# Kernel optimization log

Measured on AMD Instinct MI355X. Metric: run time of the kernel, lower is better.

## Reference

```python
import jax, jax.numpy as jnp
import numpy as np
import math

B, T, C, H = 2, 4096, 512, 8
HD = C // H


def setup_inputs() -> dict:
    key = jax.random.key(0)
    k1, k2, k3 = jax.random.split(key, 3)
    x = jax.random.normal(k1, (B, T, C), dtype=jnp.float32)
    # weights stored as [in, out] so y = x @ W (equivalent to torch Linear with W^T)
    w_qkv = jax.random.normal(k2, (C, 3 * C), dtype=jnp.float32) * (1.0 / math.sqrt(C))
    w_out = jax.random.normal(k3, (C, C), dtype=jnp.float32) * (1.0 / math.sqrt(C))
    return {"x": x, "w_qkv": w_qkv, "w_out": w_out}


def reference(x, w_qkv, w_out):
    Bs, Ts, Cs = x.shape
    qkv = x @ w_qkv                                   # [B,T,3C]
    q, k, v = jnp.split(qkv, 3, axis=-1)
    # [B,H,T,HD]
    q = q.reshape(Bs, Ts, H, HD).transpose(0, 2, 1, 3)
    k = k.reshape(Bs, Ts, H, HD).transpose(0, 2, 1, 3)
    v = v.reshape(Bs, Ts, H, HD).transpose(0, 2, 1, 3)
    scores = jnp.einsum("bhqd,bhkd->bhqk", q, k) / math.sqrt(HD)
    causal = jnp.tril(jnp.ones((Ts, Ts), dtype=bool))
    scores = jnp.where(causal[None, None], scores, -jnp.inf)
    attn = jax.nn.softmax(scores, axis=-1)            # [B,H,T,T]
    out = jnp.einsum("bhqk,bhkd->bhqd", attn, v)      # [B,H,T,HD]
    out = out.transpose(0, 2, 1, 3).reshape(Bs, Ts, Cs)
    return out @ w_out
```

## Files before the change

### kernel.cpp

```cpp
#include <hip/hip_runtime.h>
#include <hip/hip_bf16.h>

typedef __bf16 bf16;
typedef __bf16 bf16x4 __attribute__((ext_vector_type(4)));
typedef __bf16 bf16x8 __attribute__((ext_vector_type(8)));
typedef float f32x4 __attribute__((ext_vector_type(4)));

#define BB 2
#define TT 4096
#define CC 512
#define HH 8
#define HD 64
#define BHD 16
#define M_TOT 8192

#define SCL (0.125f * 1.44269504f)

#define GLDS(gptr, lptr)                                                     \
  __builtin_amdgcn_global_load_lds(                                          \
      (const __attribute__((address_space(1))) void*)(gptr),                 \
      (__attribute__((address_space(3))) void*)(lptr), 16, 0, 0)

__global__ __launch_bounds__(256) void convert_x_kernel(
    const float* __restrict__ X, bf16* __restrict__ Xb) {
  const size_t i0 = ((size_t)blockIdx.x * 256 + threadIdx.x) * 16;
  const float4* p = (const float4*)(X + i0);
#pragma unroll
  for (int c = 0; c < 2; ++c) {
    float4 a = p[c * 2], b = p[c * 2 + 1];
    bf16x8 v;
    v[0] = (bf16)a.x; v[1] = (bf16)a.y; v[2] = (bf16)a.z; v[3] = (bf16)a.w;
    v[4] = (bf16)b.x; v[5] = (bf16)b.y; v[6] = (bf16)b.z; v[7] = (bf16)b.w;
    *(bf16x8*)&Xb[i0 + c * 8] = v;
  }
}

__global__ __launch_bounds__(256) void transpose_w_kernel(
    const float* __restrict__ W, bf16* __restrict__ WT, int K, int N) {
  __shared__ float tile[64][65];
  const int n0 = blockIdx.x * 64, k0 = blockIdx.y * 64;
  const int t = threadIdx.x;
  const int rr = t >> 4, cc4 = (t & 15) * 4;
#pragma unroll
  for (int i = 0; i < 4; ++i) {
    float4 v = *(const float4*)&W[(size_t)(k0 + rr + i * 16) * N + n0 + cc4];
    tile[rr + i * 16][cc4 + 0] = v.x;
    tile[rr + i * 16][cc4 + 1] = v.y;
    tile[rr + i * 16][cc4 + 2] = v.z;
    tile[rr + i * 16][cc4 + 3] = v.w;
  }
  __syncthreads();
#pragma unroll
  for (int i = 0; i < 4; ++i) {
    const int nn = rr + i * 16;
    bf16x4 o;
#pragma unroll
    for (int j = 0; j < 4; ++j) o[j] = (bf16)tile[cc4 + j][nn];
    *(bf16x4*)&WT[(size_t)(n0 + nn) * K + k0 + cc4] = o;
  }
}

__global__ __launch_bounds__(256) void gemm_qkv_kernel(
    const bf16* __restrict__ Xb, const bf16* __restrict__ Wt,
    bf16* __restrict__ qw, bf16* __restrict__ kw, bf16* __restrict__ vw) {
  __shared__ __align__(16) bf16 As[128 * 64];
  __shared__ __align__(16) bf16 Bs[128 * 64];
  const int tid = threadIdx.x;
  const int wid = tid >> 6, lane = tid & 63, ln = lane & 15, hi = lane >> 4;
  const int wr = wid >> 1, wc = wid & 1;
  const int m0 = blockIdx.x * 128, n0 = blockIdx.y * 128;
  const int srow = lane >> 3, srcc = (lane & 7) ^ srow;

  f32x4 acc[4][4] = {};

  for (int k0 = 0; k0 < 512; k0 += 64) {
    __syncthreads();
#pragma unroll
    for (int i = 0; i < 4; ++i) {
      const int rb = 32 * wid + 8 * i;
      GLDS(&Xb[(size_t)(m0 + rb + srow) * 512 + k0 + srcc * 8], &As[rb * 64]);
      GLDS(&Wt[(size_t)(n0 + rb + srow) * 512 + k0 + srcc * 8], &Bs[rb * 64]);
    }
    __syncthreads();

    bf16x8 af[4][2], bfr[4][2];
#pragma unroll
    for (int mi = 0; mi < 4; ++mi) {
      const int row = wr * 64 + mi * 16 + ln, rs = row & 7;
      af[mi][0] = *(const bf16x8*)&As[row * 64 + ((hi ^ rs) * 8)];
      af[mi][1] = *(const bf16x8*)&As[row * 64 + (((4 + hi) ^ rs) * 8)];
    }
#pragma unroll
    for (int ni = 0; ni < 4; ++ni) {
      const int row = wc * 64 + ni * 16 + ln, rs = row & 7;
      bfr[ni][0] = *(const bf16x8*)&Bs[row * 64 + ((hi ^ rs) * 8)];
      bfr[ni][1] = *(const bf16x8*)&Bs[row * 64 + (((4 + hi) ^ rs) * 8)];
    }
#pragma unroll
    for (int mi = 0; mi < 4; ++mi)
#pragma unroll
      for (int ni = 0; ni < 4; ++ni) {
        acc[mi][ni] = __builtin_amdgcn_mfma_f32_16x16x32_bf16(af[mi][0], bfr[ni][0], acc[mi][ni], 0, 0, 0);
        acc[mi][ni] = __builtin_amdgcn_mfma_f32_16x16x32_bf16(af[mi][1], bfr[ni][1], acc[mi][ni], 0, 0, 0);
      }
  }

#pragma unroll
  for (int mi = 0; mi < 4; ++mi) {
    int rowb = m0 + wr * 64 + mi * 16 + hi * 4;
    int b = rowb >> 12, t0 = rowb & 4095;
#pragma unroll
    for (int ni = 0; ni < 4; ++ni) {
      int n = n0 + wc * 64 + ni * 16 + ln;
      int which = n >> 9, c = n & 511, h = c >> 6, d = c & 63;
      if (which == 2) {
        bf16x4 pv;
#pragma unroll
        for (int r = 0; r < 4; ++r) pv[r] = (bf16)acc[mi][ni][r];
        *(bf16x4*)&vw[((size_t)(b * HH + h) * HD + d) * TT + t0] = pv;
      } else {
        bf16* dst = which ? kw : qw;
        const float sc = which ? 1.0f : SCL;
#pragma unroll
        for (int r = 0; r < 4; ++r)
          dst[((size_t)(b * HH + h) * TT + t0 + r) * HD + d] = (bf16)(acc[mi][ni][r] * sc);
      }
    }
  }
}

__global__ __launch_bounds__(256) void attn_piece_kernel(
    const bf16* __restrict__ qw, const bf16* __restrict__ kw,
    const bf16* __restrict__ vt,
    bf16* __restrict__ po, float* __restrict__ pl) {
  __shared__ __align__(16) bf16 Ks[2][64 * 64];
  __shared__ __align__(16) bf16 Vs[2][64 * 64];
  const int tid = threadIdx.x;
  const int wid = tid >> 6, lane = tid & 63, ln = lane & 15, hi = lane >> 4;

  const int pid = blockIdx.x;
  const int pair = pid >> 1, half = pid & 1;
  const int qb = 63 - (pair >> 4);
  const int bh = pair & 15;
  const int ntot = qb + 1;
  const int h0 = (ntot + 1) >> 1;
  const int t0 = half ? h0 : 0;
  const int t1 = half ? ntot : h0;

  if (t0 >= t1) {
    for (int i = tid; i < 4096; i += 256) po[(size_t)pid * 4096 + i] = (bf16)0.f;
    if (tid < 64) pl[pid * 64 + tid] = 0.f;
    return;
  }

  const int q0w = qb * 64 + wid * 16;

  const int lrow8 = lane >> 3, lch = lane & 7;
  const int srcch = lch ^ lrow8;
  const int rbase = 8 * wid + lrow8;
  const size_t kb = (size_t)bh * TT * HD, vb = (size_t)bh * HD * TT;

  bf16x8 qf[2];
#pragma unroll
  for (int h = 0; h < 2; ++h)
    qf[h] = *(const bf16x8*)&qw[((size_t)bh * TT + q0w + ln) * HD + h * 32 + hi * 8];

  f32x4 o[4] = {};
  f32x4 osum = {};

  bf16x8 vones;
#pragma unroll
  for (int j = 0; j < 8; ++j) vones[j] = (bf16)1.0f;

#define STAGE(kv_, dstbuf) do {                                              \
    GLDS(kw + kb + (size_t)((kv_) + rbase) * HD + srcch * 8,                 \
         &Ks[dstbuf][(8 * wid) * 64]);                                       \
    GLDS(kw + kb + (size_t)((kv_) + 32 + rbase) * HD + srcch * 8,            \
         &Ks[dstbuf][(32 + 8 * wid) * 64]);                                  \
    GLDS(vt + vb + (size_t)rbase * TT + (kv_) + srcch * 8,                   \
         &Vs[dstbuf][(8 * wid) * 64]);                                       \
    GLDS(vt + vb + (size_t)(32 + rbase) * TT + (kv_) + srcch * 8,            \
         &Vs[dstbuf][(32 + 8 * wid) * 64]);                                  \
  } while (0)

#define TILE(t_, BUF) do {                                                   \
    const int kv0 = (t_) * 64;                                               \
    if ((t_) + 1 < t1) STAGE(kv0 + 64, (BUF) ^ 1);                           \
    f32x4 s[4];                                                              \
    __builtin_amdgcn_s_setprio(1);                                           \
    _Pragma("unroll")                                                        \
    for (int kt = 0; kt < 4; ++kt) {                                         \
      const int krow = kt * 16 + ln;                                         \
      const bf16* kbase = &Ks[BUF][krow * 64];                               \
      bf16x8 kf0 = *(const bf16x8*)&kbase[(hi ^ (ln & 7)) * 8];              \
      bf16x8 kf1 = *(const bf16x8*)&kbase[((4 + hi) ^ (ln & 7)) * 8];        \
      f32x4 a = {};                                                          \
      a = __builtin_amdgcn_mfma_f32_16x16x32_bf16(kf0, qf[0], a, 0, 0, 0);   \
      a = __builtin_amdgcn_mfma_f32_16x16x32_bf16(kf1, qf[1], a, 0, 0, 0);   \
      s[kt] = a;                                                             \
    }                                                                        \
    __builtin_amdgcn_s_setprio(0);                                           \
    if ((t_) == qb) {                                                        \
      const int qg = q0w + ln;                                               \
      _Pragma("unroll")                                                      \
      for (int kt = 0; kt < 4; ++kt)                                         \
        _Pragma("unroll")                                                    \
        for (int r = 0; r < 4; ++r)                                          \
          if (kv0 + kt * 16 + hi * 4 + r > qg) s[kt][r] = -1e30f;            \
    }                                                                        \
    _Pragma("unroll")                                                        \
    for (int kt = 0; kt < 4; ++kt)                                           \
      _Pragma("unroll")                                                      \
      for (int r = 0; r < 4; ++r) s[kt][r] = exp2f(s[kt][r]);                \
    bf16x8 pa[2];                                                            \
    _Pragma("unroll")                                                        \
    for (int h2 = 0; h2 < 2; ++h2)                                           \
      _Pragma("unroll")                                                      \
      for (int j = 0; j < 8; ++j)                                            \
        pa[h2][j] = (bf16)s[h2 * 2 + (j >> 2)][j & 3];                       \
    const bf16* vbase = Vs[BUF];                                             \
    __builtin_amdgcn_s_setprio(1);                                           \
    osum = __builtin_amdgcn_mfma_f32_16x16x32_bf16(pa[0], vones, osum, 0, 0, 0); \
    osum = __builtin_amdgcn_mfma_f32_16x16x32_bf16(pa[1], vones, osum, 0, 0, 0); \
    _Pragma("unroll")                                                        \
    for (int db = 0; db < 4; ++db) {                                         \
      const int d = db * 16 + ln, rowb = d * 64, dx = d & 7;                 \
      _Pragma("unroll")                                                      \
      for (int h2 = 0; h2 < 2; ++h2) {                                       \
        const int c1 = h2 * 4 + (hi >> 1);                                   \
        bf16x4 lo = *(const bf16x4*)&vbase[rowb + ((c1 ^ dx) * 8) + (hi & 1) * 4]; \
        bf16x4 hi4 = *(const bf16x4*)&vbase[rowb + (((c1 + 2) ^ dx) * 8) + (hi & 1) * 4]; \
        bf16x8 vf = __builtin_shufflevector(lo, hi4, 0, 1, 2, 3, 4, 5, 6, 7); \
        o[db] = __builtin_amdgcn_mfma_f32_16x16x32_bf16(pa[h2], vf, o[db], 0, 0, 0); \
      }                                                                      \
    }                                                                        \
    __builtin_amdgcn_s_setprio(0);                                           \
    __syncthreads();                                                         \
  } while (0)

  STAGE(t0 * 64, 0);
  __syncthreads();

  int t = t0;
  for (; t + 1 < t1; t += 2) { TILE(t, 0); TILE(t + 1, 1); }
  if (t < t1) TILE(t, 0);

  {
    bf16* ob = po + (size_t)pid * 4096;
#pragma unroll
    for (int db = 0; db < 4; ++db)
#pragma unroll
      for (int r = 0; r < 4; ++r)
        ob[(wid * 16 + hi * 4 + r) * 64 + db * 16 + ln] = (bf16)o[db][r];
    if (ln == 0) {
#pragma unroll
      for (int r = 0; r < 4; ++r)
        pl[pid * 64 + wid * 16 + hi * 4 + r] = osum[r];
    }
  }
#undef TILE
#undef STAGE
}

__global__ __launch_bounds__(256) void attn_combine_kernel(
    const bf16* __restrict__ po, const float* __restrict__ pl,
    bf16* __restrict__ aw) {
  const int cb = blockIdx.x;
  const int qb = 63 - (cb >> 4), bh = cb & 15;
  const int tid = threadIdx.x;
  const int q_ = tid >> 2, dc = (tid & 3) * 16;
  const int pg0 = cb * 2, pg1 = pg0 + 1;

  const float inv = 1.0f / (pl[pg0 * 64 + q_] + pl[pg1 * 64 + q_]);

  const bf16* o0 = po + (size_t)pg0 * 4096 + q_ * 64 + dc;
  const bf16* o1 = po + (size_t)pg1 * 4096 + q_ * 64 + dc;
  bf16* dst = aw + ((size_t)bh * TT + qb * 64 + q_) * 64 + dc;

#pragma unroll
  for (int c = 0; c < 2; ++c) {
    bf16x8 x = *(const bf16x8*)&o0[c * 8];
    bf16x8 y = *(const bf16x8*)&o1[c * 8];
    bf16x8 outv;
#pragma unroll
    for (int j = 0; j < 8; ++j)
      outv[j] = (bf16)(((float)x[j] + (float)y[j]) * inv);
    *(bf16x8*)&dst[c * 8] = outv;
  }
}

__global__ __launch_bounds__(256) void gemm_out_kernel(
    const bf16* __restrict__ A, const bf16* __restrict__ Wot,
    float* __restrict__ out) {
  __shared__ __align__(16) bf16 As[128 * 64];
  __shared__ __align__(16) bf16 Bs[64 * 64];
  const int tid = threadIdx.x;
  const int wid = tid >> 6, lane = tid & 63, ln = lane & 15, hi = lane >> 4;
  const int wr = wid >> 1, wc = wid & 1;
  const int m0 = blockIdx.x * 128, n0 = blockIdx.y * 64;
  const int srow = lane >> 3, srcc = (lane & 7) ^ srow;

  f32x4 acc[4][2] = {};

  for (int k0 = 0; k0 < 512; k0 += 64) {
    const int h = k0 >> 6;
    __syncthreads();
#pragma unroll
    for (int i = 0; i < 4; ++i) {
      const int rb = 32 * wid + 8 * i;
      const int m = m0 + rb + srow;
      const int b = m >> 12, t = m & 4095;
      GLDS(&A[((size_t)(b * HH + h) * TT + t) * HD + srcc * 8], &As[rb * 64]);
    }
#pragma unroll
    for (int i = 0; i < 2; ++i) {
      const int rb = 16 * wid + 8 * i;
      GLDS(&Wot[(size_t)(n0 + rb + srow) * 512 + k0 + srcc * 8], &Bs[rb * 64]);
    }
    __syncthreads();

    bf16x8 af[4][2], bfr[2][2];
#pragma unroll
    for (int mi = 0; mi < 4; ++mi) {
      const int row = wr * 64 + mi * 16 + ln, rs = row & 7;
      af[mi][0] = *(const bf16x8*)&As[row * 64 + ((hi ^ rs) * 8)];
      af[mi][1] = *(const bf16x8*)&As[row * 64 + (((4 + hi) ^ rs) * 8)];
    }
#pragma unroll
    for (int ni = 0; ni < 2; ++ni) {
      const int row = wc * 32 + ni * 16 + ln, rs = row & 7;
      bfr[ni][0] = *(const bf16x8*)&Bs[row * 64 + ((hi ^ rs) * 8)];
      bfr[ni][1] = *(const bf16x8*)&Bs[row * 64 + (((4 + hi) ^ rs) * 8)];
    }
#pragma unroll
    for (int mi = 0; mi < 4; ++mi)
#pragma unroll
      for (int ni = 0; ni < 2; ++ni) {
        acc[mi][ni] = __builtin_amdgcn_mfma_f32_16x16x32_bf16(af[mi][0], bfr[ni][0], acc[mi][ni], 0, 0, 0);
        acc[mi][ni] = __builtin_amdgcn_mfma_f32_16x16x32_bf16(af[mi][1], bfr[ni][1], acc[mi][ni], 0, 0, 0);
      }
  }

#pragma unroll
  for (int mi = 0; mi < 4; ++mi) {
    int rowb = m0 + wr * 64 + mi * 16 + hi * 4;
#pragma unroll
    for (int ni = 0; ni < 2; ++ni) {
      int n = n0 + wc * 32 + ni * 16 + ln;
#pragma unroll
      for (int r = 0; r < 4; ++r)
        out[(size_t)(rowb + r) * 512 + n] = acc[mi][ni][r];
    }
  }
}

extern "C" void kernel_launch(void* const* d_in, const int* in_sizes, int n_in,
                              void* d_out, int out_size, void* d_ws, size_t ws_size,
                              hipStream_t stream) {
  const float* x = (const float*)d_in[0];
  const float* w_qkv = (const float*)d_in[1];
  const float* w_out = (const float*)d_in[2];
  float* out = (float*)d_out;

  const size_t QKV_ELEMS = (size_t)BHD * TT * HD;
  bf16* qw = (bf16*)d_ws;
  bf16* kw = qw + QKV_ELEMS;
  bf16* vw = kw + QKV_ELEMS;
  bf16* aw = vw + QKV_ELEMS;
  bf16* po = aw + QKV_ELEMS;
  float* pl = (float*)(po + (size_t)2048 * 4096);
  bf16* wqt = (bf16*)(pl + (size_t)2048 * 64);
  bf16* wot = wqt + (size_t)1536 * 512;
  bf16* xb = po;

  convert_x_kernel<<<1024, 256, 0, stream>>>(x, xb);
  transpose_w_kernel<<<dim3(1536 / 64, 512 / 64), 256, 0, stream>>>(w_qkv, wqt, 512, 1536);
  transpose_w_kernel<<<dim3(512 / 64, 512 / 64), 256, 0, stream>>>(w_out, wot, 512, 512);
  gemm_qkv_kernel<<<dim3(M_TOT / 128, 1536 / 128), 256, 0, stream>>>(xb, wqt, qw, kw, vw);
  attn_piece_kernel<<<2048, 256, 0, stream>>>(qw, kw, vw, po, pl);
  attn_combine_kernel<<<1024, 256, 0, stream>>>(po, pl, aw);
  gemm_out_kernel<<<dim3(M_TOT / 128, 512 / 64), 256, 0, stream>>>(aw, wot, out);
}
```

Baseline: 122.1 us.

## Split attention into fixed 16-tile KV chunks and merge weight transposes

```diff
diff --git a/kernel.cpp b/kernel.cpp
--- a/kernel.cpp
+++ b/kernel.cpp
@@ -16,6 +16,12 @@
 
 #define SCL (0.125f * 1.44269504f)
 
+#if __has_builtin(__builtin_amdgcn_exp2f)
+#define EXP2F(x) __builtin_amdgcn_exp2f(x)
+#else
+#define EXP2F(x) exp2f(x)
+#endif
+
 #define GLDS(gptr, lptr)                                                     \
   __builtin_amdgcn_global_load_lds(                                          \
       (const __attribute__((address_space(1))) void*)(gptr),                 \
@@ -36,9 +42,13 @@
 }
 
 __global__ __launch_bounds__(256) void transpose_w_kernel(
-    const float* __restrict__ W, bf16* __restrict__ WT, int K, int N) {
+    const float* __restrict__ Wq, const float* __restrict__ Wo,
+    bf16* __restrict__ WQT, bf16* __restrict__ WOT) {
   __shared__ float tile[64][65];
-  const int n0 = blockIdx.x * 64, k0 = blockIdx.y * 64;
+  int b = blockIdx.x;
+  const float* W; bf16* WT; int N, n0, k0;
+  if (b < 192) { W = Wq; WT = WQT; N = 1536; n0 = (b % 24) * 64; k0 = (b / 24) * 64; }
+  else { b -= 192; W = Wo; WT = WOT; N = 512; n0 = (b & 7) * 64; k0 = (b >> 3) * 64; }
   const int t = threadIdx.x;
   const int rr = t >> 4, cc4 = (t & 15) * 4;
 #pragma unroll
@@ -56,7 +66,7 @@
     bf16x4 o;
 #pragma unroll
     for (int j = 0; j < 4; ++j) o[j] = (bf16)tile[cc4 + j][nn];
-    *(bf16x4*)&WT[(size_t)(n0 + nn) * K + k0 + cc4] = o;
+    *(bf16x4*)&WT[(size_t)(n0 + nn) * 512 + k0 + cc4] = o;
   }
 }
 
@@ -138,20 +148,17 @@
   const int tid = threadIdx.x;
   const int wid = tid >> 6, lane = tid & 63, ln = lane & 15, hi = lane >> 4;
 
+  int qb, bh, chunk;
+  {
+    const int pid = blockIdx.x;
+    if (pid < 1024)      { qb = 63 - (pid >> 6); int r = pid & 63;  bh = r >> 2; chunk = r & 3; }
+    else if (pid < 1792) { int l = pid - 1024; qb = 47 - l / 48; int r = l % 48; bh = r / 3; chunk = r % 3; }
+    else if (pid < 2304) { int l = pid - 1792; qb = 31 - (l >> 5); int r = l & 31; bh = r >> 1; chunk = r & 1; }
+    else                 { int l = pid - 2304; qb = 15 - (l >> 4); bh = l & 15; chunk = 0; }
+  }
+  const int t0 = chunk * 16;
+  const int t1 = (t0 + 16 < qb + 1) ? (t0 + 16) : (qb + 1);
   const int pid = blockIdx.x;
-  const int pair = pid >> 1, half = pid & 1;
-  const int qb = 63 - (pair >> 4);
-  const int bh = pair & 15;
-  const int ntot = qb + 1;
-  const int h0 = (ntot + 1) >> 1;
-  const int t0 = half ? h0 : 0;
-  const int t1 = half ? ntot : h0;
-
-  if (t0 >= t1) {
-    for (int i = tid; i < 4096; i += 256) po[(size_t)pid * 4096 + i] = (bf16)0.f;
-    if (tid < 64) pl[pid * 64 + tid] = 0.f;
-    return;
-  }
 
   const int q0w = qb * 64 + wid * 16;
 
@@ -165,6 +172,25 @@
   for (int h = 0; h < 2; ++h)
     qf[h] = *(const bf16x8*)&qw[((size_t)bh * TT + q0w + ln) * HD + h * 32 + hi * 8];
 
+  const bf16* kp[4][2];
+#pragma unroll
+  for (int kt = 0; kt < 4; ++kt) {
+    const int krow = kt * 16 + ln;
+    kp[kt][0] = &Ks[0][krow * 64 + ((hi ^ (ln & 7)) * 8)];
+    kp[kt][1] = &Ks[0][krow * 64 + (((4 + hi) ^ (ln & 7)) * 8)];
+  }
+  const bf16* vp[4][2][2];
+#pragma unroll
+  for (int db = 0; db < 4; ++db) {
+    const int d = db * 16 + ln, rowb = d * 64, dx = d & 7;
+#pragma unroll
+    for (int h2 = 0; h2 < 2; ++h2) {
+      const int c1 = h2 * 4 + (hi >> 1);
+      vp[db][h2][0] = &Vs[0][rowb + ((c1 ^ dx) * 8) + (hi & 1) * 4];
+      vp[db][h2][1] = &Vs[0][rowb + (((c1 + 2) ^ dx) * 8) + (hi & 1) * 4];
+    }
+  }
+
   f32x4 o[4] = {};
   f32x4 osum = {};
 
@@ -172,28 +198,34 @@
 #pragma unroll
   for (int j = 0; j < 8; ++j) vones[j] = (bf16)1.0f;
 
-#define STAGE(kv_, dstbuf) do {                                              \
-    GLDS(kw + kb + (size_t)((kv_) + rbase) * HD + srcch * 8,                 \
-         &Ks[dstbuf][(8 * wid) * 64]);                                       \
-    GLDS(kw + kb + (size_t)((kv_) + 32 + rbase) * HD + srcch * 8,            \
-         &Ks[dstbuf][(32 + 8 * wid) * 64]);                                  \
-    GLDS(vt + vb + (size_t)rbase * TT + (kv_) + srcch * 8,                   \
-         &Vs[dstbuf][(8 * wid) * 64]);                                       \
-    GLDS(vt + vb + (size_t)(32 + rbase) * TT + (kv_) + srcch * 8,            \
-         &Vs[dstbuf][(32 + 8 * wid) * 64]);                                  \
-  } while (0)
+  {
+    const int kv = t0 * 64;
+    GLDS(kw + kb + (size_t)(kv + rbase) * HD + srcch * 8, &Ks[0][(8 * wid) * 64]);
+    GLDS(kw + kb + (size_t)(kv + 32 + rbase) * HD + srcch * 8, &Ks[0][(32 + 8 * wid) * 64]);
+    GLDS(vt + vb + (size_t)rbase * TT + kv + srcch * 8, &Vs[0][(8 * wid) * 64]);
+    GLDS(vt + vb + (size_t)(32 + rbase) * TT + kv + srcch * 8, &Vs[0][(32 + 8 * wid) * 64]);
+  }
+  const bf16* pk0 = kw + kb + (size_t)((t0 + 1) * 64 + rbase) * HD + srcch * 8;
+  const bf16* pk1 = pk0 + (size_t)32 * HD;
+  const bf16* pv0 = vt + vb + (size_t)rbase * TT + (t0 + 1) * 64 + srcch * 8;
+  const bf16* pv1 = pv0 + (size_t)32 * TT;
+  __syncthreads();
 
 #define TILE(t_, BUF) do {                                                   \
     const int kv0 = (t_) * 64;                                               \
-    if ((t_) + 1 < t1) STAGE(kv0 + 64, (BUF) ^ 1);                           \
+    if ((t_) + 1 < t1) {                                                     \
+      GLDS(pk0, &Ks[(BUF) ^ 1][(8 * wid) * 64]);                             \
+      GLDS(pk1, &Ks[(BUF) ^ 1][(32 + 8 * wid) * 64]);                        \
+      GLDS(pv0, &Vs[(BUF) ^ 1][(8 * wid) * 64]);                             \
+      GLDS(pv1, &Vs[(BUF) ^ 1][(32 + 8 * wid) * 64]);                        \
+      pk0 += (size_t)64 * HD; pk1 += (size_t)64 * HD; pv0 += 64; pv1 += 64;  \
+    }                                                                        \
     f32x4 s[4];                                                              \
     __builtin_amdgcn_s_setprio(1);                                           \
     _Pragma("unroll")                                                        \
     for (int kt = 0; kt < 4; ++kt) {                                         \
-      const int krow = kt * 16 + ln;                                         \
-      const bf16* kbase = &Ks[BUF][krow * 64];                               \
-      bf16x8 kf0 = *(const bf16x8*)&kbase[(hi ^ (ln & 7)) * 8];              \
-      bf16x8 kf1 = *(const bf16x8*)&kbase[((4 + hi) ^ (ln & 7)) * 8];        \
+      bf16x8 kf0 = *(const bf16x8*)(kp[kt][0] + (BUF) * 4096);               \
+      bf16x8 kf1 = *(const bf16x8*)(kp[kt][1] + (BUF) * 4096);               \
       f32x4 a = {};                                                          \
       a = __builtin_amdgcn_mfma_f32_16x16x32_bf16(kf0, qf[0], a, 0, 0, 0);   \
       a = __builtin_amdgcn_mfma_f32_16x16x32_bf16(kf1, qf[1], a, 0, 0, 0);   \
@@ -211,25 +243,22 @@
     _Pragma("unroll")                                                        \
     for (int kt = 0; kt < 4; ++kt)                                           \
       _Pragma("unroll")                                                      \
-      for (int r = 0; r < 4; ++r) s[kt][r] = exp2f(s[kt][r]);                \
+      for (int r = 0; r < 4; ++r) s[kt][r] = EXP2F(s[kt][r]);                \
     bf16x8 pa[2];                                                            \
     _Pragma("unroll")                                                        \
     for (int h2 = 0; h2 < 2; ++h2)                                           \
       _Pragma("unroll")                                                      \
       for (int j = 0; j < 8; ++j)                                            \
         pa[h2][j] = (bf16)s[h2 * 2 + (j >> 2)][j & 3];                       \
-    const bf16* vbase = Vs[BUF];                                             \
     __builtin_amdgcn_s_setprio(1);                                           \
     osum = __builtin_amdgcn_mfma_f32_16x16x32_bf16(pa[0], vones, osum, 0, 0, 0); \
     osum = __builtin_amdgcn_mfma_f32_16x16x32_bf16(pa[1], vones, osum, 0, 0, 0); \
     _Pragma("unroll")                                                        \
     for (int db = 0; db < 4; ++db) {                                         \
-      const int d = db * 16 + ln, rowb = d * 64, dx = d & 7;                 \
       _Pragma("unroll")                                                      \
       for (int h2 = 0; h2 < 2; ++h2) {                                       \
-        const int c1 = h2 * 4 + (hi >> 1);                                   \
-        bf16x4 lo = *(const bf16x4*)&vbase[rowb + ((c1 ^ dx) * 8) + (hi & 1) * 4]; \
-        bf16x4 hi4 = *(const bf16x4*)&vbase[rowb + (((c1 + 2) ^ dx) * 8) + (hi & 1) * 4]; \
+        bf16x4 lo = *(const bf16x4*)(vp[db][h2][0] + (BUF) * 4096);          \
+        bf16x4 hi4 = *(const bf16x4*)(vp[db][h2][1] + (BUF) * 4096);         \
         bf16x8 vf = __builtin_shufflevector(lo, hi4, 0, 1, 2, 3, 4, 5, 6, 7); \
         o[db] = __builtin_amdgcn_mfma_f32_16x16x32_bf16(pa[h2], vf, o[db], 0, 0, 0); \
       }                                                                      \
@@ -238,9 +267,6 @@
     __syncthreads();                                                         \
   } while (0)
 
-  STAGE(t0 * 64, 0);
-  __syncthreads();
-
   int t = t0;
   for (; t + 1 < t1; t += 2) { TILE(t, 0); TILE(t + 1, 1); }
   if (t < t1) TILE(t, 0);
@@ -259,7 +285,6 @@
     }
   }
 #undef TILE
-#undef STAGE
 }
 
 __global__ __launch_bounds__(256) void attn_combine_kernel(
@@ -269,23 +294,33 @@
   const int qb = 63 - (cb >> 4), bh = cb & 15;
   const int tid = threadIdx.x;
   const int q_ = tid >> 2, dc = (tid & 3) * 16;
-  const int pg0 = cb * 2, pg1 = pg0 + 1;
-
-  const float inv = 1.0f / (pl[pg0 * 64 + q_] + pl[pg1 * 64 + q_]);
-
-  const bf16* o0 = po + (size_t)pg0 * 4096 + q_ * 64 + dc;
-  const bf16* o1 = po + (size_t)pg1 * 4096 + q_ * 64 + dc;
+
+  const int nch = (qb >> 4) + 1;
+  const int base = (qb >= 48) ? 0 : (qb >= 32) ? 1024 : (qb >= 16) ? 1792 : 2304;
+  const int top  = (qb >= 48) ? 63 : (qb >= 32) ? 47 : (qb >= 16) ? 31 : 15;
+  const int p0 = base + (top - qb) * 16 * nch + bh * nch;
+
+  float sum = 0.f;
+  for (int c = 0; c < nch; ++c) sum += pl[(p0 + c) * 64 + q_];
+  const float inv = 1.0f / sum;
+
+  float acc[16] = {};
+  for (int c = 0; c < nch; ++c) {
+    const bf16* ob = po + (size_t)(p0 + c) * 4096 + q_ * 64 + dc;
+#pragma unroll
+    for (int cc = 0; cc < 2; ++cc) {
+      bf16x8 x = *(const bf16x8*)&ob[cc * 8];
+#pragma unroll
+      for (int j = 0; j < 8; ++j) acc[cc * 8 + j] += (float)x[j];
+    }
+  }
   bf16* dst = aw + ((size_t)bh * TT + qb * 64 + q_) * 64 + dc;
-
-#pragma unroll
-  for (int c = 0; c < 2; ++c) {
-    bf16x8 x = *(const bf16x8*)&o0[c * 8];
-    bf16x8 y = *(const bf16x8*)&o1[c * 8];
+#pragma unroll
+  for (int cc = 0; cc < 2; ++cc) {
     bf16x8 outv;
 #pragma unroll
-    for (int j = 0; j < 8; ++j)
-      outv[j] = (bf16)(((float)x[j] + (float)y[j]) * inv);
-    *(bf16x8*)&dst[c * 8] = outv;
+    for (int j = 0; j < 8; ++j) outv[j] = (bf16)(acc[cc * 8 + j] * inv);
+    *(bf16x8*)&dst[cc * 8] = outv;
   }
 }
 
@@ -368,16 +403,15 @@
   bf16* vw = kw + QKV_ELEMS;
   bf16* aw = vw + QKV_ELEMS;
   bf16* po = aw + QKV_ELEMS;
-  float* pl = (float*)(po + (size_t)2048 * 4096);
-  bf16* wqt = (bf16*)(pl + (size_t)2048 * 64);
+  float* pl = (float*)(po + (size_t)2560 * 4096);
+  bf16* wqt = (bf16*)(pl + (size_t)2560 * 64);
   bf16* wot = wqt + (size_t)1536 * 512;
   bf16* xb = po;
 
   convert_x_kernel<<<1024, 256, 0, stream>>>(x, xb);
-  transpose_w_kernel<<<dim3(1536 / 64, 512 / 64), 256, 0, stream>>>(w_qkv, wqt, 512, 1536);
-  transpose_w_kernel<<<dim3(512 / 64, 512 / 64), 256, 0, stream>>>(w_out, wot, 512, 512);
+  transpose_w_kernel<<<256, 256, 0, stream>>>(w_qkv, w_out, wqt, wot);
   gemm_qkv_kernel<<<dim3(M_TOT / 128, 1536 / 128), 256, 0, stream>>>(xb, wqt, qw, kw, vw);
-  attn_piece_kernel<<<2048, 256, 0, stream>>>(qw, kw, vw, po, pl);
+  attn_piece_kernel<<<2560, 256, 0, stream>>>(qw, kw, vw, po, pl);
   attn_combine_kernel<<<1024, 256, 0, stream>>>(po, pl, aw);
   gemm_out_kernel<<<dim3(M_TOT / 128, 512 / 64), 256, 0, stream>>>(aw, wot, out);
 }
```

Result: faster. 115.5 us (-5.4%).
